# Kernel tuning notes

Measured on AMD Instinct MI355X. Metric: run time of the kernel, lower is better.

## Reference

```python
import jax, jax.numpy as jnp
import numpy as np

N_NODES = 50000
N_EDGES = 600000
D = 128
EPS = 1e-5
AVG_D_LOG = float(np.log(4 + 1))  # avg_d={'log': log(avg_d+1)}, avg_d=4


def setup_inputs() -> dict:
    key = jax.random.key(0)
    ks = jax.random.split(key, 8)
    h = jax.random.normal(ks[0], (N_NODES, D), dtype=jnp.float32)
    # guarantee every node has at least one incoming edge (self-loop)
    edge_dst = jnp.concatenate([
        jnp.arange(N_NODES, dtype=jnp.int64),
        jax.random.randint(ks[1], (N_EDGES - N_NODES,), 0, N_NODES).astype(jnp.int64),
    ])
    edge_src = jax.random.randint(ks[2], (N_EDGES,), 0, N_NODES).astype(jnp.int64)
    def lin(k, fan_in, fan_out):
        lim = 1.0 / np.sqrt(fan_in)
        return jax.random.uniform(k, (fan_in, fan_out), jnp.float32, -lim, lim)
    W_pre = lin(ks[3], 2 * D, D)
    b_pre = jnp.zeros((D,), jnp.float32)
    W_post = lin(ks[4], 12 * D + D, D)  # 4 aggregators * 3 scalers * D + in_dim
    b_post = jnp.zeros((D,), jnp.float32)
    W_mix = lin(ks[5], D, D)
    b_mix = jnp.zeros((D,), jnp.float32)
    return {"h": h, "edge_src": edge_src, "edge_dst": edge_dst,
            "W_pre": W_pre, "b_pre": b_pre, "W_post": W_post,
            "b_post": b_post, "W_mix": W_mix, "b_mix": b_mix}


def reference(h, edge_src, edge_dst, W_pre, b_pre, W_post, b_post, W_mix, b_mix):
    n = h.shape[0]
    # pretrans_edges: cat(src, dst) -> Linear -> ReLU (MLP act) -> ReLU (outer)
    z2 = jnp.concatenate([h[edge_src], h[edge_dst]], axis=1)        # [E, 2D]
    e = jax.nn.relu(z2 @ W_pre + b_pre)                             # [E, D]
    # multi-aggregator segment reduce over destination nodes
    deg = jax.ops.segment_sum(jnp.ones_like(edge_dst, jnp.float32), edge_dst, n)  # [N]
    inv_deg = 1.0 / deg[:, None]
    mean = jax.ops.segment_sum(e, edge_dst, n) * inv_deg
    mean_sq = jax.ops.segment_sum(e * e, edge_dst, n) * inv_deg
    std = jnp.sqrt(jax.nn.relu(mean_sq - mean * mean) + EPS)
    mx = jax.ops.segment_max(e, edge_dst, n)
    mn = jax.ops.segment_min(e, edge_dst, n)
    agg = jnp.concatenate([mean, mx, mn, std], axis=1)              # [N, 4D]
    # scalers: identity, amplification, attenuation
    log_d = jnp.log(deg + 1.0)[:, None]
    scaled = jnp.concatenate([agg, agg * (log_d / AVG_D_LOG), agg * (AVG_D_LOG / log_d)], axis=1)  # [N, 12D]
    # posttrans: cat(h, aggregated) -> Linear -> ReLU
    hp = jax.nn.relu(jnp.concatenate([h, scaled], axis=1) @ W_post + b_post)  # [N, D]
    # mixing network + residual (node_dim == out_dim)
    out = h + jax.nn.leaky_relu(hp @ W_mix + b_mix, negative_slope=0.01)
    return out
```

## Files before the change

### kernel.cpp

```cpp
#include <hip/hip_runtime.h>
#include <hip/hip_bf16.h>

#define N_NODES 50000
#define N_EDGES 600000
#define D 128
#define NB_SCAN 196

constexpr float AVG_D_LOG = 1.6094379124341003f;
constexpr float EPS_V = 1e-5f;

#define PQ_B     0ul
#define AGG_B    25600000ul
#define HBF_B    76800000ul
#define WPRET2_B 89600000ul
#define WPOSTT_B 89665536ul
#define WMIXT_B  90091520ul
#define DEGC_B   90124288ul
#define OFF_B    90324288ul
#define CUR_B    90524352ul
#define SRCS_B   90724352ul
#define BSUM_B   93124352ul

typedef __attribute__((ext_vector_type(8))) short bf16x8;
typedef __attribute__((ext_vector_type(4))) float f32x4;

__device__ __forceinline__ short f2b(float f) {
    unsigned u = __builtin_bit_cast(unsigned, f);
    u += 0x7fffu + ((u >> 16) & 1u);
    return (short)(u >> 16);
}
__device__ __forceinline__ unsigned pk2(float a, float b) {
    return (unsigned)(unsigned short)f2b(a) | ((unsigned)(unsigned short)f2b(b) << 16);
}
__device__ __forceinline__ float blo(unsigned u) { return __uint_as_float(u << 16); }
__device__ __forceinline__ float bhi(unsigned u) { return __uint_as_float(u & 0xffff0000u); }

__device__ __forceinline__ void gld_lds16(const void* g, void* l) {
    __builtin_amdgcn_global_load_lds(
        (const __attribute__((address_space(1))) void*)g,
        (__attribute__((address_space(3))) void*)l, 16, 0, 0);
}

__global__ __launch_bounds__(256) void prep_kernel(
    const float* __restrict__ h, const float* __restrict__ Wpre,
    const float* __restrict__ Wpost, const float* __restrict__ Wmix,
    short* __restrict__ hbf, short* __restrict__ wpreT2,
    short* __restrict__ wpostT, short* __restrict__ wmixT,
    int* __restrict__ degc, int* __restrict__ cursor)
{
    long i = (long)blockIdx.x * 256 + threadIdx.x;
    if (i < 6400000) { hbf[i] = f2b(h[i]); return; }
    i -= 6400000;
    if (i < 32768) {
        int n = i >> 7, k = i & 127;
        float v = (n < 128) ? Wpre[k * 128 + n] : Wpre[(k + 128) * 128 + (n - 128)];
        wpreT2[n * 128 + k] = f2b(v);
        return;
    }
    i -= 32768;
    if (i < 212992) { int k = i >> 7, n = i & 127; wpostT[n * 1664 + k] = f2b(Wpost[k * 128 + n]); return; }
    i -= 212992;
    if (i < 16384) { int k = i >> 7, n = i & 127; wmixT[n * 128 + k] = f2b(Wmix[k * 128 + n]); return; }
    i -= 16384;
    if (i < N_NODES) { degc[i] = 0; return; }
    i -= N_NODES;
    if (i < N_NODES) cursor[i] = 0;
}

__global__ __launch_bounds__(256) void hist_kernel(const int* __restrict__ edst, int* __restrict__ degc) {
    int e = blockIdx.x * 256 + threadIdx.x;
    if (e < N_EDGES) atomicAdd(&degc[edst[e]], 1);
}

__global__ __launch_bounds__(256) void scan1_kernel(const int* __restrict__ degc, int* __restrict__ bsum) {
    int n = blockIdx.x * 256 + threadIdx.x;
    int v = (n < N_NODES) ? degc[n] : 0;
#pragma unroll
    for (int o = 32; o > 0; o >>= 1) v += __shfl_down(v, o);
    __shared__ int w4[4];
    if ((threadIdx.x & 63) == 0) w4[threadIdx.x >> 6] = v;
    __syncthreads();
    if (threadIdx.x == 0) bsum[blockIdx.x] = w4[0] + w4[1] + w4[2] + w4[3];
}

__global__ __launch_bounds__(256) void scan2_kernel(int* __restrict__ bsum, int* __restrict__ off) {
    __shared__ int sd[256];
    int tid = threadIdx.x;
    int v = (tid < NB_SCAN) ? bsum[tid] : 0;
    sd[tid] = v;
    __syncthreads();
    for (int o = 1; o < 256; o <<= 1) {
        int t = (tid >= o) ? sd[tid - o] : 0;
        __syncthreads();
        sd[tid] += t;
        __syncthreads();
    }
    if (tid < NB_SCAN) bsum[tid] = sd[tid] - v;
    if (tid == 0) off[N_NODES] = sd[255];
}

__global__ __launch_bounds__(256) void scan3_kernel(const int* __restrict__ degc,
                                                    const int* __restrict__ bsum, int* __restrict__ off) {
    __shared__ int sd[256];
    int tid = threadIdx.x;
    int n = blockIdx.x * 256 + tid;
    int v = (n < N_NODES) ? degc[n] : 0;
    sd[tid] = v;
    __syncthreads();
    for (int o = 1; o < 256; o <<= 1) {
        int t = (tid >= o) ? sd[tid - o] : 0;
        __syncthreads();
        sd[tid] += t;
        __syncthreads();
    }
    if (n < N_NODES) off[n] = sd[tid] - v + bsum[blockIdx.x];
}

__global__ __launch_bounds__(256) void scatter_kernel(const int* __restrict__ esrc, const int* __restrict__ edst,
                                                      const int* __restrict__ off, int* __restrict__ cursor,
                                                      int* __restrict__ srcs) {
    int e = blockIdx.x * 256 + threadIdx.x;
    if (e < N_EDGES) {
        int d = edst[e];
        int p = off[d] + atomicAdd(&cursor[d], 1);
        srcs[p] = esrc[e];
    }
}

__global__ __launch_bounds__(256) void gemm_pq_kernel(
    const short* __restrict__ hbf, const short* __restrict__ wpreT2,
    const float* __restrict__ bpre, short* __restrict__ PQ)
{
    __shared__ __align__(16) short As[128][72];
    __shared__ __align__(16) short Bs[128][72];

    const int tid = threadIdx.x;
    const int cg = blockIdx.x & 1;
    const int bn = (blockIdx.x >> 1) * 128;
    const int lane = tid & 63, wv = tid >> 6;
    const int lm = lane & 15, quad = lane >> 4;

    f32x4 acc[2][8];
#pragma unroll
    for (int a = 0; a < 2; a++)
#pragma unroll
        for (int b = 0; b < 8; b++) acc[a][b] = (f32x4){0.f, 0.f, 0.f, 0.f};

#pragma unroll
    for (int kc = 0; kc < 2; kc++) {
        __syncthreads();
#pragma unroll
        for (int t = 0; t < 4; t++) {
            int q = tid + t * 256;
            int m = q >> 3, seg = q & 7;
            int n = bn + m; if (n >= N_NODES) n = N_NODES - 1;
            *(int4*)&As[m][seg * 8] = *(const int4*)(hbf + (long)n * 128 + kc * 64 + seg * 8);
        }
#pragma unroll
        for (int t = 0; t < 4; t++) {
            int q = tid + t * 256;
            int n = q >> 3, seg = q & 7;
            *(int4*)&Bs[n][seg * 8] = *(const int4*)(wpreT2 + (cg * 128 + n) * 128 + kc * 64 + seg * 8);
        }
        __syncthreads();
#pragma unroll
        for (int ks = 0; ks < 2; ks++) {
            const int ko = ks * 32 + quad * 8;
            bf16x8 a0 = *(const bf16x8*)&As[wv * 32 + lm][ko];
            bf16x8 a1 = *(const bf16x8*)&As[wv * 32 + 16 + lm][ko];
#pragma unroll
            for (int ct = 0; ct < 8; ct++) {
                bf16x8 b = *(const bf16x8*)&Bs[ct * 16 + lm][ko];
                acc[0][ct] = __builtin_amdgcn_mfma_f32_16x16x32_bf16(b, a0, acc[0][ct], 0, 0, 0);
                acc[1][ct] = __builtin_amdgcn_mfma_f32_16x16x32_bf16(b, a1, acc[1][ct], 0, 0, 0);
            }
        }
    }

#pragma unroll
    for (int rt = 0; rt < 2; rt++) {
        int row = wv * 32 + rt * 16 + lm;
        int n = bn + row;
        if (n >= N_NODES) continue;
        short* dst = PQ + (long)n * 256;
#pragma unroll
        for (int ct = 0; ct < 8; ct++) {
            int col = cg * 128 + ct * 16 + quad * 4;
            float v0 = acc[rt][ct][0], v1 = acc[rt][ct][1], v2 = acc[rt][ct][2], v3 = acc[rt][ct][3];
            if (cg) {
                float4 bv = *(const float4*)(bpre + (col - 128));
                v0 += bv.x; v1 += bv.y; v2 += bv.z; v3 += bv.w;
            }
            int2 pkd; pkd.x = (int)pk2(v0, v1); pkd.y = (int)pk2(v2, v3);
            *(int2*)(dst + col) = pkd;
        }
    }
}

__global__ __launch_bounds__(256) void edgestats_kernel(
    const short* __restrict__ PQ, const int* __restrict__ srcs,
    const int* __restrict__ off, short* __restrict__ aggbf)
{
    const int wv = threadIdx.x >> 6, lane = threadIdx.x & 63;
    const int n = blockIdx.x * 4 + wv;
    const unsigned* Pb = (const unsigned*)PQ;

    const int s0 = __builtin_amdgcn_readfirstlane(off[n]);
    const int s1 = __builtin_amdgcn_readfirstlane(off[n + 1]);

    unsigned qu = Pb[(long)n * 128 + 64 + lane];
    const float qa = blo(qu), qb = bhi(qu);

    float sA = 0.f, sB = 0.f, qA = 0.f, qB = 0.f;
    float mxA = -1e30f, mxB = -1e30f, mnA = 1e30f, mnB = 1e30f;

    int p = s0;
    for (; p + 4 <= s1; p += 4) {
        int i0 = srcs[p], i1 = srcs[p + 1], i2 = srcs[p + 2], i3 = srcs[p + 3];
        unsigned u0 = Pb[(long)i0 * 128 + lane];
        unsigned u1 = Pb[(long)i1 * 128 + lane];
        unsigned u2 = Pb[(long)i2 * 128 + lane];
        unsigned u3 = Pb[(long)i3 * 128 + lane];
#pragma unroll
        for (int j = 0; j < 4; j++) {
            unsigned u = (j == 0) ? u0 : (j == 1) ? u1 : (j == 2) ? u2 : u3;
            float a = blo(u) + qa; a = a > 0.f ? a : 0.f;
            float b = bhi(u) + qb; b = b > 0.f ? b : 0.f;
            sA += a; sB += b; qA += a * a; qB += b * b;
            mxA = fmaxf(mxA, a); mxB = fmaxf(mxB, b);
            mnA = fminf(mnA, a); mnB = fminf(mnB, b);
        }
    }
    for (; p < s1; p++) {
        unsigned u = Pb[(long)srcs[p] * 128 + lane];
        float a = blo(u) + qa; a = a > 0.f ? a : 0.f;
        float b = bhi(u) + qb; b = b > 0.f ? b : 0.f;
        sA += a; sB += b; qA += a * a; qB += b * b;
        mxA = fmaxf(mxA, a); mxB = fmaxf(mxB, b);
        mnA = fminf(mnA, a); mnB = fminf(mnB, b);
    }

    float inv = 1.0f / (float)(s1 - s0);
    float mA = sA * inv, mB = sB * inv;
    float vA = qA * inv - mA * mA; vA = vA > 0.f ? vA : 0.f;
    float vB = qB * inv - mB * mB; vB = vB > 0.f ? vB : 0.f;
    float stA = sqrtf(vA + EPS_V), stB = sqrtf(vB + EPS_V);

    unsigned* ag = (unsigned*)(aggbf + (long)n * 512);
    ag[lane]       = pk2(mA, mB);
    ag[64 + lane]  = pk2(mxA, mxB);
    ag[128 + lane] = pk2(mnA, mnB);
    ag[192 + lane] = pk2(stA, stB);
}


__device__ __forceinline__ void stageA_t(short* ldsT, const short* src, int rs, int co,
                                         int bn, int wv, int lane) {
    const int sub = lane >> 3, seg = lane & 7;
    const int sg = (seg ^ sub) * 8;
#pragma unroll
    for (int t = 0; t < 4; t++) {
        int i = wv * 4 + t;
        int row = i * 8 + sub;
        int n = bn + row; if (n >= N_NODES) n = N_NODES - 1;
        gld_lds16(src + (long)n * rs + co + sg, ldsT + i * 512);
    }
}
__device__ __forceinline__ void stageB_t(short* ldsT, const short* src, int rs, int co,
                                         int wv, int lane) {
    const int sub = lane >> 3, seg = lane & 7;
    const int sg = (seg ^ sub) * 8;
#pragma unroll
    for (int t = 0; t < 4; t++) {
        int i = wv * 4 + t;
        int row = i * 8 + sub;
        gld_lds16(src + (long)row * rs + co + sg, ldsT + i * 512);
    }
}

#define MFMA_ITER(AB, BB, ACC)                                                      \
    {                                                                               \
        _Pragma("unroll")                                                           \
        for (int ks = 0; ks < 2; ks++) {                                            \
            const int qx = (((ks * 4 + quad) ^ r7) * 8);                            \
            bf16x8 a0 = *(const bf16x8*)&(AB)[(wv * 32 + lm) * 64 + qx];            \
            bf16x8 a1 = *(const bf16x8*)&(AB)[(wv * 32 + 16 + lm) * 64 + qx];       \
            _Pragma("unroll")                                                       \
            for (int ct = 0; ct < 8; ct++) {                                        \
                bf16x8 b = *(const bf16x8*)&(BB)[(ct * 16 + lm) * 64 + qx];         \
                ACC[0][ct] = __builtin_amdgcn_mfma_f32_16x16x32_bf16(b, a0, ACC[0][ct], 0, 0, 0); \
                ACC[1][ct] = __builtin_amdgcn_mfma_f32_16x16x32_bf16(b, a1, ACC[1][ct], 0, 0, 0); \
            }                                                                       \
        }                                                                           \
    }

__global__ __launch_bounds__(256, 2) void node_kernel(
    const float* __restrict__ h, const short* __restrict__ hbf, const short* __restrict__ aggbf,
    const int* __restrict__ degc, const short* __restrict__ wpostT, const float* __restrict__ bpost,
    const short* __restrict__ wmixT, const float* __restrict__ bmix, float* __restrict__ out)
{
    __shared__ __align__(16) short As[2][8192];
    __shared__ __align__(16) short Bs[2][8192];
    __shared__ float sAmp[128], sAtt[128];

    const int tid = threadIdx.x;
    const int bn = blockIdx.x * 128;
    const int lane = tid & 63, wv = tid >> 6;
    const int lm = lane & 15, quad = lane >> 4;
    const int r7 = lm & 7;

    if (tid < 128) {
        int n = bn + tid; if (n >= N_NODES) n = N_NODES - 1;
        float d = (float)degc[n];
        float ld = logf(d + 1.0f);
        sAmp[tid] = ld * (1.0f / AVG_D_LOG);
        sAtt[tid] = AVG_D_LOG / ld;
    }

    f32x4 accI[2][8], accM[2][8], accT[2][8];
#pragma unroll
    for (int a = 0; a < 2; a++)
#pragma unroll
        for (int b = 0; b < 8; b++) {
            accI[a][b] = (f32x4){0.f, 0.f, 0.f, 0.f};
            accM[a][b] = (f32x4){0.f, 0.f, 0.f, 0.f};
            accT[a][b] = (f32x4){0.f, 0.f, 0.f, 0.f};
        }


    stageA_t(As[0], hbf, 128, 0, bn, wv, lane);
    stageB_t(Bs[0], wpostT, 1664, 0, wv, lane);
    __syncthreads();

    stageA_t(As[1], hbf, 128, 64, bn, wv, lane);
    stageB_t(Bs[1], wpostT, 1664, 64, wv, lane);
    MFMA_ITER(As[0], Bs[0], accI);
    __syncthreads();

    stageA_t(As[0], aggbf, 512, 0, bn, wv, lane);
    stageB_t(Bs[0], wpostT, 1664, 2 * 64, wv, lane);
    MFMA_ITER(As[1], Bs[1], accI);
    __syncthreads();

    int pb = 0;
    for (int j = 0; j < 8; j++) {
        short* Ac = As[j & 1];
        if (j < 7) {
            int jn = j + 1;
            stageA_t(As[jn & 1], aggbf, 512, (jn >> 1) * 128 + (jn & 1) * 64, bn, wv, lane);
        }
        stageB_t(Bs[pb ^ 1], wpostT, 1664, (10 + j) * 64, wv, lane);
        MFMA_ITER(Ac, Bs[pb], accI);
        __syncthreads();

        stageB_t(Bs[pb], wpostT, 1664, (18 + j) * 64, wv, lane);
        MFMA_ITER(Ac, Bs[pb ^ 1], accM);
        __syncthreads();

        if (j < 7) stageB_t(Bs[pb ^ 1], wpostT, 1664, (3 + j) * 64, wv, lane);
        MFMA_ITER(Ac, Bs[pb], accT);
        __syncthreads();
        pb ^= 1;
    }

    stageB_t(Bs[0], wmixT, 128, 0, wv, lane);
    stageB_t(Bs[1], wmixT, 128, 64, wv, lane);

    const float am0 = sAmp[wv * 32 + lm],      at0 = sAtt[wv * 32 + lm];
    const float am1 = sAmp[wv * 32 + 16 + lm], at1 = sAtt[wv * 32 + 16 + lm];
#pragma unroll
    for (int rt = 0; rt < 2; rt++) {
        const float am = rt ? am1 : am0, at = rt ? at1 : at0;
        const int row = wv * 32 + rt * 16 + lm;
#pragma unroll
        for (int ct = 0; ct < 8; ct++) {
            float4 bv = *(const float4*)(bpost + ct * 16 + quad * 4);
            float v0 = accI[rt][ct][0] + am * accM[rt][ct][0] + at * accT[rt][ct][0] + bv.x;
            float v1 = accI[rt][ct][1] + am * accM[rt][ct][1] + at * accT[rt][ct][1] + bv.y;
            float v2 = accI[rt][ct][2] + am * accM[rt][ct][2] + at * accT[rt][ct][2] + bv.z;
            float v3 = accI[rt][ct][3] + am * accM[rt][ct][3] + at * accT[rt][ct][3] + bv.w;
            v0 = v0 > 0.f ? v0 : 0.f; v1 = v1 > 0.f ? v1 : 0.f;
            v2 = v2 > 0.f ? v2 : 0.f; v3 = v3 > 0.f ? v3 : 0.f;
            int2 pkd; pkd.x = (int)pk2(v0, v1); pkd.y = (int)pk2(v2, v3);
            const int cb = (ct & 3) * 32 + quad * 8;
            const int sb = ((((cb >> 4) ^ r7) << 4) | (cb & 15));
            *(int2*)((char*)As[ct >> 2] + row * 128 + sb) = pkd;
        }
    }
    __syncthreads();

    f32x4 accO[2][8];
#pragma unroll
    for (int a = 0; a < 2; a++)
#pragma unroll
        for (int b = 0; b < 8; b++) accO[a][b] = (f32x4){0.f, 0.f, 0.f, 0.f};
#pragma unroll
    for (int kc = 0; kc < 2; kc++) {
        MFMA_ITER(As[kc], Bs[kc], accO);
    }

#pragma unroll
    for (int rt = 0; rt < 2; rt++) {
        int row = wv * 32 + rt * 16 + lm;
        int n = bn + row;
        if (n >= N_NODES) continue;
#pragma unroll
        for (int ct = 0; ct < 8; ct++) {
            int col = ct * 16 + quad * 4;
            float4 bv = *(const float4*)(bmix + col);
            float4 hv = *(const float4*)(h + (long)n * 128 + col);
            float4 o;
            float v0 = accO[rt][ct][0] + bv.x; v0 = v0 > 0.f ? v0 : 0.01f * v0; o.x = hv.x + v0;
            float v1 = accO[rt][ct][1] + bv.y; v1 = v1 > 0.f ? v1 : 0.01f * v1; o.y = hv.y + v1;
            float v2 = accO[rt][ct][2] + bv.z; v2 = v2 > 0.f ? v2 : 0.01f * v2; o.z = hv.z + v2;
            float v3 = accO[rt][ct][3] + bv.w; v3 = v3 > 0.f ? v3 : 0.01f * v3; o.w = hv.w + v3;
            *(float4*)(out + (long)n * 128 + col) = o;
        }
    }
}

extern "C" void kernel_launch(void* const* d_in, const int* in_sizes, int n_in,
                              void* d_out, int out_size, void* d_ws, size_t ws_size,
                              hipStream_t stream) {
    const float* h     = (const float*)d_in[0];
    const int*   esrc  = (const int*)d_in[1];
    const int*   edst  = (const int*)d_in[2];
    const float* Wpre  = (const float*)d_in[3];
    const float* bpre  = (const float*)d_in[4];
    const float* Wpost = (const float*)d_in[5];
    const float* bpost = (const float*)d_in[6];
    const float* Wmix  = (const float*)d_in[7];
    const float* bmix  = (const float*)d_in[8];
    float* out = (float*)d_out;
    char* ws = (char*)d_ws;

    short* PQ     = (short*)(ws + PQ_B);
    short* aggbf  = (short*)(ws + AGG_B);
    short* hbf    = (short*)(ws + HBF_B);
    short* wpreT2 = (short*)(ws + WPRET2_B);
    short* wpostT = (short*)(ws + WPOSTT_B);
    short* wmixT  = (short*)(ws + WMIXT_B);
    int*   degc   = (int*)(ws + DEGC_B);
    int*   off    = (int*)(ws + OFF_B);
    int*   cursor = (int*)(ws + CUR_B);
    int*   srcs   = (int*)(ws + SRCS_B);
    int*   bsum   = (int*)(ws + BSUM_B);

    prep_kernel<<<26415, 256, 0, stream>>>(h, Wpre, Wpost, Wmix, hbf, wpreT2, wpostT, wmixT, degc, cursor);
    hist_kernel<<<(N_EDGES + 255) / 256, 256, 0, stream>>>(edst, degc);
    scan1_kernel<<<NB_SCAN, 256, 0, stream>>>(degc, bsum);
    scan2_kernel<<<1, 256, 0, stream>>>(bsum, off);
    scan3_kernel<<<NB_SCAN, 256, 0, stream>>>(degc, bsum, off);
    scatter_kernel<<<(N_EDGES + 255) / 256, 256, 0, stream>>>(esrc, edst, off, cursor, srcs);
    gemm_pq_kernel<<<((N_NODES + 127) / 128) * 2, 256, 0, stream>>>(hbf, wpreT2, bpre, PQ);
    edgestats_kernel<<<N_NODES / 4, 256, 0, stream>>>(PQ, srcs, off, aggbf);
    node_kernel<<<(N_NODES + 127) / 128, 256, 0, stream>>>(h, hbf, aggbf, degc, wpostT, bpost, wmixT, bmix, out);
}
```

Measured before the change: 266.6 us.

## Vectorize h conversion, deepen edge gather unroll, and use counted waits in node GEMM

The prep kernel now converts h to bf16 eight floats per thread with vector loads and stores, cutting its thread count. The edge-stats gather loop is unrolled to eight edges so more independent loads are in flight. In the node kernel, full __syncthreads are replaced by explicit vmcnt waits plus raw barriers, so the next tile's global-to-LDS loads stay in flight across the barrier. The wmix prefetch is also folded into the last loop iteration. The hand-counted vmcnt values must exactly match the number of outstanding loads per stage, or the kernel will read stale shared memory.

```diff
diff --git a/kernel.cpp b/kernel.cpp
--- a/kernel.cpp
+++ b/kernel.cpp
@@ -41,6 +41,18 @@
         (__attribute__((address_space(3))) void*)l, 16, 0, 0);
 }
 
+#define WAIT_BAR(N) do {                                              \
+    asm volatile("s_waitcnt vmcnt(" #N ")" ::: "memory");             \
+    __builtin_amdgcn_sched_barrier(0);                                \
+    __builtin_amdgcn_s_barrier();                                     \
+    __builtin_amdgcn_sched_barrier(0);                                \
+} while (0)
+#define BAR_ONLY() do {                                               \
+    __builtin_amdgcn_sched_barrier(0);                                \
+    __builtin_amdgcn_s_barrier();                                     \
+    __builtin_amdgcn_sched_barrier(0);                                \
+} while (0)
+
 __global__ __launch_bounds__(256) void prep_kernel(
     const float* __restrict__ h, const float* __restrict__ Wpre,
     const float* __restrict__ Wpost, const float* __restrict__ Wmix,
@@ -49,8 +61,16 @@
     int* __restrict__ degc, int* __restrict__ cursor)
 {
     long i = (long)blockIdx.x * 256 + threadIdx.x;
-    if (i < 6400000) { hbf[i] = f2b(h[i]); return; }
-    i -= 6400000;
+    if (i < 800000) {
+        float4 a = *(const float4*)(h + i * 8);
+        float4 b = *(const float4*)(h + i * 8 + 4);
+        int4 v;
+        v.x = (int)pk2(a.x, a.y); v.y = (int)pk2(a.z, a.w);
+        v.z = (int)pk2(b.x, b.y); v.w = (int)pk2(b.z, b.w);
+        *(int4*)(hbf + i * 8) = v;
+        return;
+    }
+    i -= 800000;
     if (i < 32768) {
         int n = i >> 7, k = i & 127;
         float v = (n < 128) ? Wpre[k * 128 + n] : Wpre[(k + 128) * 128 + (n - 128)];
@@ -66,6 +86,7 @@
     i -= N_NODES;
     if (i < N_NODES) cursor[i] = 0;
 }
+#define PREP_BLOCKS ((800000 + 32768 + 212992 + 16384 + 2 * N_NODES + 255) / 256)
 
 __global__ __launch_bounds__(256) void hist_kernel(const int* __restrict__ edst, int* __restrict__ degc) {
     int e = blockIdx.x * 256 + threadIdx.x;
@@ -215,17 +236,17 @@
     float mxA = -1e30f, mxB = -1e30f, mnA = 1e30f, mnB = 1e30f;
 
     int p = s0;
-    for (; p + 4 <= s1; p += 4) {
-        int i0 = srcs[p], i1 = srcs[p + 1], i2 = srcs[p + 2], i3 = srcs[p + 3];
-        unsigned u0 = Pb[(long)i0 * 128 + lane];
-        unsigned u1 = Pb[(long)i1 * 128 + lane];
-        unsigned u2 = Pb[(long)i2 * 128 + lane];
-        unsigned u3 = Pb[(long)i3 * 128 + lane];
-#pragma unroll
-        for (int j = 0; j < 4; j++) {
-            unsigned u = (j == 0) ? u0 : (j == 1) ? u1 : (j == 2) ? u2 : u3;
-            float a = blo(u) + qa; a = a > 0.f ? a : 0.f;
-            float b = bhi(u) + qb; b = b > 0.f ? b : 0.f;
+    for (; p + 8 <= s1; p += 8) {
+        int idx[8];
+#pragma unroll
+        for (int j = 0; j < 8; j++) idx[j] = srcs[p + j];
+        unsigned u[8];
+#pragma unroll
+        for (int j = 0; j < 8; j++) u[j] = Pb[(long)idx[j] * 128 + lane];
+#pragma unroll
+        for (int j = 0; j < 8; j++) {
+            float a = blo(u[j]) + qa; a = a > 0.f ? a : 0.f;
+            float b = bhi(u[j]) + qb; b = b > 0.f ? b : 0.f;
             sA += a; sB += b; qA += a * a; qB += b * b;
             mxA = fmaxf(mxA, a); mxB = fmaxf(mxB, b);
             mnA = fminf(mnA, a); mnB = fminf(mnB, b);
@@ -316,6 +337,7 @@
         sAmp[tid] = ld * (1.0f / AVG_D_LOG);
         sAtt[tid] = AVG_D_LOG / ld;
     }
+    __syncthreads();
 
     f32x4 accI[2][8], accM[2][8], accT[2][8];
 #pragma unroll
@@ -330,40 +352,46 @@
 
     stageA_t(As[0], hbf, 128, 0, bn, wv, lane);
     stageB_t(Bs[0], wpostT, 1664, 0, wv, lane);
-    __syncthreads();
 
     stageA_t(As[1], hbf, 128, 64, bn, wv, lane);
     stageB_t(Bs[1], wpostT, 1664, 64, wv, lane);
+    WAIT_BAR(8);
     MFMA_ITER(As[0], Bs[0], accI);
-    __syncthreads();
-
+    BAR_ONLY();
+
+    stageB_t(Bs[0], wpostT, 1664, 2 * 64, wv, lane);
     stageA_t(As[0], aggbf, 512, 0, bn, wv, lane);
-    stageB_t(Bs[0], wpostT, 1664, 2 * 64, wv, lane);
+    WAIT_BAR(8);
     MFMA_ITER(As[1], Bs[1], accI);
-    __syncthreads();
+    BAR_ONLY();
 
     int pb = 0;
     for (int j = 0; j < 8; j++) {
         short* Ac = As[j & 1];
+        stageB_t(Bs[pb ^ 1], wpostT, 1664, (10 + j) * 64, wv, lane);
         if (j < 7) {
             int jn = j + 1;
             stageA_t(As[jn & 1], aggbf, 512, (jn >> 1) * 128 + (jn & 1) * 64, bn, wv, lane);
-        }
-        stageB_t(Bs[pb ^ 1], wpostT, 1664, (10 + j) * 64, wv, lane);
+            WAIT_BAR(8);
+        } else {
+            WAIT_BAR(4);
+        }
         MFMA_ITER(Ac, Bs[pb], accI);
-        __syncthreads();
+        BAR_ONLY();
 
         stageB_t(Bs[pb], wpostT, 1664, (18 + j) * 64, wv, lane);
+        if (j < 7) { WAIT_BAR(8); } else { WAIT_BAR(4); }
         MFMA_ITER(Ac, Bs[pb ^ 1], accM);
-        __syncthreads();
+        BAR_ONLY();
 
         if (j < 7) stageB_t(Bs[pb ^ 1], wpostT, 1664, (3 + j) * 64, wv, lane);
+        else       stageB_t(Bs[pb ^ 1], wmixT, 128, 0, wv, lane);
+        WAIT_BAR(4);
         MFMA_ITER(Ac, Bs[pb], accT);
-        __syncthreads();
+        BAR_ONLY();
         pb ^= 1;
     }
 
-    stageB_t(Bs[0], wmixT, 128, 0, wv, lane);
     stageB_t(Bs[1], wmixT, 128, 64, wv, lane);
 
     const float am0 = sAmp[wv * 32 + lm],      at0 = sAtt[wv * 32 + lm];
@@ -446,7 +474,7 @@
     int*   srcs   = (int*)(ws + SRCS_B);
     int*   bsum   = (int*)(ws + BSUM_B);
 
-    prep_kernel<<<26415, 256, 0, stream>>>(h, Wpre, Wpost, Wmix, hbf, wpreT2, wpostT, wmixT, degc, cursor);
+    prep_kernel<<<PREP_BLOCKS, 256, 0, stream>>>(h, Wpre, Wpost, Wmix, hbf, wpreT2, wpostT, wmixT, degc, cursor);
     hist_kernel<<<(N_EDGES + 255) / 256, 256, 0, stream>>>(edst, degc);
     scan1_kernel<<<NB_SCAN, 256, 0, stream>>>(degc, bsum);
     scan2_kernel<<<1, 256, 0, stream>>>(bsum, off);
```

New measurement: 259.9 us. 2.5% less time.
